# Optimization experiments

Hardware: AMD Instinct MI355X
Metric: run time of the kernel (lower is better)

Reference implementation:

```python
import jax, jax.numpy as jnp
import numpy as np

NEG = -1e9  # effectively -inf for masked logits, grad-safe

def apply_rope(t, cos, sin):
    # t: [b, H, S, D]; cos/sin: [S, D] -> rotate-half RoPE
    d = t.shape[-1]
    t1, t2 = t[..., : d // 2], t[..., d // 2 :]
    rot = jnp.concatenate([-t2, t1], axis=-1)
    return t * cos[None, None] + rot * sin[None, None]


def setup_inputs() -> dict:
    key = jax.random.key(0)
    ks = jax.random.split(key, 8)
    b, S, d_in = 1, 4096, 2048
    H, G, D = 16, 4, 128
    d_out = H * D
    sc = 1.0 / np.sqrt(d_in)
    x = jax.random.normal(ks[0], (b, S, d_in), dtype=jnp.float32)
    # causal mask: True = masked (future positions)
    mask = jnp.triu(jnp.ones((S, S), dtype=bool), k=1)
    inv = 1.0 / (10000.0 ** (jnp.arange(0, D, 2, dtype=jnp.float32) / D))
    ang = jnp.arange(S, dtype=jnp.float32)[:, None] * inv[None, :]  # [S, D/2]
    ang = jnp.concatenate([ang, ang], axis=-1)                      # [S, D]
    cos, sin = jnp.cos(ang), jnp.sin(ang)
    Wq = jax.random.normal(ks[1], (d_out, d_in), dtype=jnp.float32) * sc
    Wk = jax.random.normal(ks[2], (G * D, d_in), dtype=jnp.float32) * sc
    Wv = jax.random.normal(ks[3], (G * D, d_in), dtype=jnp.float32) * sc
    Wo = jax.random.normal(ks[4], (d_in, d_out), dtype=jnp.float32) * sc
    return {"x": x, "mask": mask, "cos": cos, "sin": sin,
            "Wq": Wq, "Wk": Wk, "Wv": Wv, "Wo": Wo}


def reference(x, mask, cos, sin, Wq, Wk, Wv, Wo):
    b, S, d_in = x.shape
    G = Wk.shape[0] // cos.shape[-1]          # num_kv_groups
    D = cos.shape[-1]                          # head_dim
    H = Wq.shape[0] // D                       # num_heads
    n = H // G                                 # group_size
    q = (x @ Wq.T).reshape(b, S, H, D).transpose(0, 2, 1, 3)   # [b,H,S,D]
    k = (x @ Wk.T).reshape(b, S, G, D).transpose(0, 2, 1, 3)   # [b,G,S,D]
    v = (x @ Wv.T).reshape(b, S, G, D).transpose(0, 2, 1, 3)
    q = apply_rope(q, cos, sin)
    k = apply_rope(k, cos, sin)
    # GQA: group heads instead of repeat_interleave (head h -> group h // n)
    qg = q.reshape(b, G, n, S, D)
    scores = jnp.einsum('bgnqd,bgkd->bgnqk', qg, k)            # [b,G,n,S,S]
    scores = jnp.where(mask[None, None, None], NEG, scores)
    w = jax.nn.softmax(scores / np.sqrt(D), axis=-1)
    ctx = jnp.einsum('bgnqk,bgkd->bgnqd', w, v)                # [b,G,n,S,D]
    ctx = ctx.reshape(b, H, S, D).transpose(0, 2, 1, 3).reshape(b, S, H * D)
    return ctx @ Wo.T
```

## Files before the change

kernel.cpp:

```cpp
#include <hip/hip_runtime.h>

typedef __attribute__((ext_vector_type(8))) short bf16x8;
typedef __attribute__((ext_vector_type(4))) short bf16x4;
typedef __attribute__((ext_vector_type(8))) unsigned short u16x8;
typedef __attribute__((ext_vector_type(4))) float f32x4;

__device__ __forceinline__ unsigned short f2b(float f) {
  unsigned int u = __builtin_bit_cast(unsigned int, f);
  u += 0x7FFFu + ((u >> 16) & 1u);
  return (unsigned short)(u >> 16);
}
__device__ __forceinline__ float b2f(unsigned short h) {
  return __builtin_bit_cast(float, ((unsigned int)h) << 16);
}

__device__ __forceinline__ f32x4 mfma16x16x16(bf16x4 a, bf16x4 b, f32x4 c) {
#if __has_builtin(__builtin_amdgcn_mfma_f32_16x16x16bf16_1k)
  return __builtin_amdgcn_mfma_f32_16x16x16bf16_1k(a, b, c, 0, 0, 0);
#else
  asm volatile("v_mfma_f32_16x16x16_bf16 %0, %1, %2, %0" : "+v"(c) : "v"(a), "v"(b));
  return c;
#endif
}

#define AS1(p) (const __attribute__((address_space(1))) void*)(p)
#define AS3(p) (__attribute__((address_space(3))) void*)(p)

__global__ __launch_bounds__(256) void k_cvt(const float* __restrict__ in,
                                             unsigned short* __restrict__ out,
                                             float scale) {
  int i = blockIdx.x * 256 + threadIdx.x;
  const float4* p = (const float4*)in + (size_t)i * 2;
  float4 a = p[0], b = p[1];
  u16x8 r;
  r[0] = f2b(a.x * scale); r[1] = f2b(a.y * scale);
  r[2] = f2b(a.z * scale); r[3] = f2b(a.w * scale);
  r[4] = f2b(b.x * scale); r[5] = f2b(b.y * scale);
  r[6] = f2b(b.z * scale); r[7] = f2b(b.w * scale);
  *((u16x8*)out + i) = r;
}

__global__ __launch_bounds__(256) void k_rope(unsigned short* __restrict__ qk,
                                              const float* __restrict__ cosb,
                                              const float* __restrict__ sinb) {
  int tid = blockIdx.x * 256 + threadIdx.x;
  int oct = tid & 7;
  int hd  = (tid >> 3) % 20;
  int s   = (tid >> 3) / 20;
  unsigned short* p1 = qk + (size_t)s * 3072 + hd * 128 + oct * 8;
  unsigned short* p2 = p1 + 64;
  u16x8 a = *(const u16x8*)p1;
  u16x8 b = *(const u16x8*)p2;
  const float4* cp = (const float4*)(cosb + (size_t)s * 128 + oct * 8);
  const float4* sp = (const float4*)(sinb + (size_t)s * 128 + oct * 8);
  float4 c0 = cp[0], c1 = cp[1], s0 = sp[0], s1 = sp[1];
  float cs[8] = {c0.x,c0.y,c0.z,c0.w,c1.x,c1.y,c1.z,c1.w};
  float sn[8] = {s0.x,s0.y,s0.z,s0.w,s1.x,s1.y,s1.z,s1.w};
  u16x8 ra, rb;
#pragma unroll
  for (int j = 0; j < 8; ++j) {
    float av = b2f(a[j]), bv = b2f(b[j]);
    ra[j] = f2b(av * cs[j] - bv * sn[j]);
    rb[j] = f2b(bv * cs[j] + av * sn[j]);
  }
  *(u16x8*)p1 = ra;
  *(u16x8*)p2 = rb;
}

__global__ __launch_bounds__(256) void k_tr(const unsigned short* __restrict__ src,
                                            unsigned short* __restrict__ dst) {
  __shared__ unsigned short tile[64][72];
  const int bs = blockIdx.x, bc = blockIdx.y, t = threadIdx.x;
#pragma unroll
  for (int i = 0; i < 2; ++i) {
    int c8 = t + 256 * i;
    int row = c8 >> 3, cb = c8 & 7;
    u16x8 v = *(const u16x8*)(src + (size_t)(bs * 64 + row) * 3072 + 2560 + bc * 64 + cb * 8);
#pragma unroll
    for (int j = 0; j < 8; ++j) tile[row][cb * 8 + j] = v[j];
  }
  __syncthreads();
#pragma unroll
  for (int i = 0; i < 2; ++i) {
    int c8 = t + 256 * i;
    int crow = c8 >> 3, sb = c8 & 7;
    u16x8 v;
#pragma unroll
    for (int j = 0; j < 8; ++j) v[j] = tile[sb * 8 + j][crow];
    *(u16x8*)(dst + (size_t)(bc * 64 + crow) * 4096 + bs * 64 + sb * 8) = v;
  }
}

template <int OUTF32>
__global__ __launch_bounds__(256) void k_gemm_bt(
    const unsigned short* __restrict__ A, const unsigned short* __restrict__ B,
    void* __restrict__ C, int K, int lda, int ldb, int ldc) {
  __shared__ unsigned short As[128 * 64];
  __shared__ unsigned short Bs[128 * 64];
  const int t = threadIdx.x;
  const int lane = t & 63, w = t >> 6;
  const int wm = w >> 1, wn = w & 1;
  const int bn = blockIdx.x, bm = blockIdx.y;
  const unsigned short* Arow = A + (size_t)(bm * 128) * lda;
  const unsigned short* Brow = B + (size_t)(bn * 128) * ldb;

  f32x4 acc[4][4] = {};
  for (int kt = 0; kt < K; kt += 64) {
#pragma unroll
    for (int i = 0; i < 4; ++i) {
      int idx = i * 256 + t;
      int r = idx >> 3, blk = idx & 7;
      int sb = blk ^ (r & 7);
      __builtin_amdgcn_global_load_lds(AS1(Arow + (size_t)r * lda + kt + sb * 8),
                                       AS3(As + (i * 256 + w * 64) * 8), 16, 0, 0);
    }
#pragma unroll
    for (int i = 0; i < 4; ++i) {
      int idx = i * 256 + t;
      int r = idx >> 3, blk = idx & 7;
      int sb = blk ^ (r & 7);
      __builtin_amdgcn_global_load_lds(AS1(Brow + (size_t)r * ldb + kt + sb * 8),
                                       AS3(Bs + (i * 256 + w * 64) * 8), 16, 0, 0);
    }
    __syncthreads();
#pragma unroll
    for (int kk = 0; kk < 2; ++kk) {
      bf16x8 av[4], bv[4];
#pragma unroll
      for (int i = 0; i < 4; ++i) {
        int r = wm * 64 + i * 16 + (lane & 15);
        int off = (r * 128 + (kk * 32 + (lane >> 4) * 8) * 2) ^ ((r & 7) << 4);
        av[i] = *(const bf16x8*)((const char*)As + off);
      }
#pragma unroll
      for (int j = 0; j < 4; ++j) {
        int r = wn * 64 + j * 16 + (lane & 15);
        int off = (r * 128 + (kk * 32 + (lane >> 4) * 8) * 2) ^ ((r & 7) << 4);
        bv[j] = *(const bf16x8*)((const char*)Bs + off);
      }
#pragma unroll
      for (int i = 0; i < 4; ++i)
#pragma unroll
        for (int j = 0; j < 4; ++j)
          acc[i][j] = __builtin_amdgcn_mfma_f32_16x16x32_bf16(av[i], bv[j], acc[i][j], 0, 0, 0);
    }
    __syncthreads();
  }
#pragma unroll
  for (int i = 0; i < 4; ++i)
#pragma unroll
    for (int j = 0; j < 4; ++j)
#pragma unroll
      for (int r = 0; r < 4; ++r) {
        int m = bm * 128 + wm * 64 + i * 16 + (lane >> 4) * 4 + r;
        int n = bn * 128 + wn * 64 + j * 16 + (lane & 15);
        float v = acc[i][j][r];
        if (OUTF32) ((float*)C)[(size_t)m * ldc + n] = v;
        else        ((unsigned short*)C)[(size_t)m * ldc + n] = f2b(v);
      }
}

__device__ __forceinline__ void stage_k(const unsigned short* __restrict__ qk,
                                        unsigned short* __restrict__ dst,
                                        int kt, int g, int t, int w) {
#pragma unroll
  for (int i = 0; i < 4; ++i) {
    int idx = i * 256 + t;
    int r = idx >> 4, blk = idx & 15;
    int sb = (blk & 8) | ((blk ^ r) & 7);
    __builtin_amdgcn_global_load_lds(
        AS1(qk + (size_t)(kt * 64 + r) * 3072 + 2048 + g * 128 + sb * 8),
        AS3(dst + (i * 256 + w * 64) * 8), 16, 0, 0);
  }
}
__device__ __forceinline__ void stage_v(const unsigned short* __restrict__ vT,
                                        unsigned short* __restrict__ dst,
                                        int kt, int g, int t, int w) {
#pragma unroll
  for (int i = 0; i < 4; ++i) {
    int idx = i * 256 + t;
    int r = idx >> 3, blk = idx & 7;
    int sb = blk ^ (r & 7);
    __builtin_amdgcn_global_load_lds(
        AS1(vT + (size_t)(g * 128 + r) * 4096 + kt * 64 + sb * 8),
        AS3(dst + (i * 256 + w * 64) * 8), 16, 0, 0);
  }
}

__global__ __launch_bounds__(256, 2) void k_attn(const unsigned short* __restrict__ qk,
                                                 const unsigned short* __restrict__ vT,
                                                 unsigned short* __restrict__ ctx) {
  __shared__ unsigned short Ks[2][64 * 128];
  __shared__ unsigned short Vs[2][64 * 128];
  const int b = blockIdx.x, h = blockIdx.y, g = h >> 2;
  const int t = threadIdx.x, lane = t & 63, w = t >> 6;
  const int l15 = lane & 15, lq = lane >> 4;

  for (int ph = 0; ph < 2; ++ph) {
    const int qt = ph ? 63 - b : b;
    const int qg = qt * 64 + w * 16 + l15;

    bf16x8 aq[4];
    {
      const unsigned short* qb =
          qk + (size_t)(qt * 64 + w * 16 + l15) * 3072 + h * 128 + lq * 8;
#pragma unroll
      for (int sl = 0; sl < 4; ++sl) aq[sl] = *(const bf16x8*)(qb + sl * 32);
    }
    f32x4 o[8] = {};
    float lsum = 0.f;

    stage_k(qk, Ks[0], 0, g, t, w);
    stage_v(vT, Vs[0], 0, g, t, w);
    asm volatile("s_waitcnt vmcnt(0)" ::: "memory");
    __builtin_amdgcn_s_barrier();

    auto tile = [&](const unsigned short* Kb, const unsigned short* Vb,
                    int kt, bool maskT) {
      f32x4 st[4] = {};
      __builtin_amdgcn_s_setprio(1);
#pragma unroll
      for (int sl = 0; sl < 4; ++sl)
#pragma unroll
        for (int nt = 0; nt < 4; ++nt) {
          int key = nt * 16 + l15;
          int off = (key * 256 + sl * 64 + lq * 16) ^ ((key & 7) << 4);
          bf16x8 bk = *(const bf16x8*)((const char*)Kb + off);
          st[nt] = __builtin_amdgcn_mfma_f32_16x16x32_bf16(bk, aq[sl], st[nt], 0, 0, 0);
        }
      __builtin_amdgcn_s_setprio(0);

      bf16x4 pa[4];
#pragma unroll
      for (int nt = 0; nt < 4; ++nt)
#pragma unroll
        for (int r = 0; r < 4; ++r) {
          float p = __builtin_amdgcn_exp2f(st[nt][r]);
          if (maskT) {
            int key = kt * 64 + nt * 16 + lq * 4 + r;
            if (key > qg) p = 0.f;
          }
          lsum += p;
          unsigned int u = __builtin_bit_cast(unsigned int, p) + 0x8000u;
          pa[nt][r] = (short)(u >> 16);
        }

      __builtin_amdgcn_s_setprio(1);
#pragma unroll
      for (int nt = 0; nt < 4; ++nt)
#pragma unroll
        for (int dt = 0; dt < 8; ++dt) {
          int d = dt * 16 + l15;
          int off = (d * 128 + nt * 32 + lq * 8) ^ ((d & 7) << 4);
          bf16x4 vv = *(const bf16x4*)((const char*)Vb + off);
          o[dt] = mfma16x16x16(pa[nt], vv, o[dt]);
        }
      __builtin_amdgcn_s_setprio(0);
    };

    for (int kt = 0; kt < qt; ++kt) {
      const int cur = kt & 1;
      stage_k(qk, Ks[cur ^ 1], kt + 1, g, t, w);
      stage_v(vT, Vs[cur ^ 1], kt + 1, g, t, w);
      tile(Ks[cur], Vs[cur], kt, false);
      asm volatile("s_waitcnt vmcnt(0)" ::: "memory");
      __builtin_amdgcn_s_barrier();
    }
    {
      const int cur = qt & 1;
      tile(Ks[cur], Vs[cur], qt, true);
      __builtin_amdgcn_s_barrier();
    }

    float fs = lsum;
    fs += __shfl_xor(fs, 16);
    fs += __shfl_xor(fs, 32);
    float invq[4];
#pragma unroll
    for (int r = 0; r < 4; ++r) invq[r] = 1.f / __shfl(fs, lq * 4 + r);
#pragma unroll
    for (int dt = 0; dt < 8; ++dt)
#pragma unroll
      for (int r = 0; r < 4; ++r) {
        int q = qt * 64 + w * 16 + lq * 4 + r;
        int c = h * 128 + dt * 16 + l15;
        ctx[(size_t)q * 2048 + c] = f2b(o[dt][r] * invq[r]);
      }
  }
}

extern "C" void kernel_launch(void* const* d_in, const int* in_sizes, int n_in,
                              void* d_out, int out_size, void* d_ws, size_t ws_size,
                              hipStream_t stream) {
  const float* x    = (const float*)d_in[0];
  const float* cosb = (const float*)d_in[2];
  const float* sinb = (const float*)d_in[3];
  const float* Wq   = (const float*)d_in[4];
  const float* Wk   = (const float*)d_in[5];
  const float* Wv   = (const float*)d_in[6];
  const float* Wo   = (const float*)d_in[7];

  char* p = (char*)d_ws;
  unsigned short* xb   = (unsigned short*)p; p += (size_t)8388608 * 2;
  unsigned short* wqkv = (unsigned short*)p; p += (size_t)6291456 * 2;
  unsigned short* Wob  = (unsigned short*)p; p += (size_t)4194304 * 2;
  unsigned short* qkvb = (unsigned short*)p; p += (size_t)4096 * 3072 * 2;
  unsigned short* vTb  = (unsigned short*)p; p += (size_t)512 * 4096 * 2;
  unsigned short* ctx  = (unsigned short*)p; p += (size_t)4096 * 2048 * 2;
  if (ws_size < (size_t)(p - (char*)d_ws)) return;

  const float SC = 0.12751741f;

  k_cvt<<<4096, 256, 0, stream>>>(x,  xb, 1.f);
  k_cvt<<<2048, 256, 0, stream>>>(Wq, wqkv,           SC);
  k_cvt<<< 512, 256, 0, stream>>>(Wk, wqkv + 4194304, 1.f);
  k_cvt<<< 512, 256, 0, stream>>>(Wv, wqkv + 5242880, 1.f);
  k_cvt<<<2048, 256, 0, stream>>>(Wo, Wob, 1.f);

  k_gemm_bt<0><<<dim3(24, 32), 256, 0, stream>>>(xb, wqkv, qkvb, 2048, 2048, 2048, 3072);

  k_rope<<<2560, 256, 0, stream>>>(qkvb, cosb, sinb);
  k_tr<<<dim3(64, 8), 256, 0, stream>>>(qkvb, vTb);

  k_attn<<<dim3(32, 16), 256, 0, stream>>>(qkvb, vTb, ctx);

  k_gemm_bt<1><<<dim3(16, 32), 256, 0, stream>>>(ctx, Wob, d_out, 2048, 2048, 2048, 2048);
}
```

Measured before the change: 255.1 us.

## Merge conversion and post-GEMM launches and streamline the attention inner loop

The five fp32-to-bf16 conversion launches become one kernel that picks its source from the block index. RoPE and the V transpose are merged into a single launch, and they touch disjoint column ranges. In attention, the K/V staging pointers and swizzled LDS offsets are computed once and then incremented each tile. Probabilities are packed with v_cvt_pk_bf16_f32, and the softmax row sum comes from an extra MFMA against a ones vector instead of scalar adds and shuffles. The aim is less launch overhead and fewer VALU instructions per tile, at the cost of one extra MFMA per key sub-tile and a row sum taken from bf16-rounded probabilities.

```diff
diff --git a/kernel.cpp b/kernel.cpp
--- a/kernel.cpp
+++ b/kernel.cpp
@@ -4,6 +4,7 @@
 typedef __attribute__((ext_vector_type(4))) short bf16x4;
 typedef __attribute__((ext_vector_type(8))) unsigned short u16x8;
 typedef __attribute__((ext_vector_type(4))) float f32x4;
+typedef __attribute__((ext_vector_type(2))) unsigned int u32x2;
 
 __device__ __forceinline__ unsigned short f2b(float f) {
   unsigned int u = __builtin_bit_cast(unsigned int, f);
@@ -23,13 +24,20 @@
 #endif
 }
 
+__device__ __forceinline__ bf16x4 pack4(float a, float b, float c, float d) {
+  unsigned int lo, hi;
+  asm("v_cvt_pk_bf16_f32 %0, %1, %2" : "=v"(lo) : "v"(a), "v"(b));
+  asm("v_cvt_pk_bf16_f32 %0, %1, %2" : "=v"(hi) : "v"(c), "v"(d));
+  u32x2 u = {lo, hi};
+  return __builtin_bit_cast(bf16x4, u);
+}
+
 #define AS1(p) (const __attribute__((address_space(1))) void*)(p)
 #define AS3(p) (__attribute__((address_space(3))) void*)(p)
 
-__global__ __launch_bounds__(256) void k_cvt(const float* __restrict__ in,
-                                             unsigned short* __restrict__ out,
-                                             float scale) {
-  int i = blockIdx.x * 256 + threadIdx.x;
+__device__ __forceinline__ void cvt8(const float* __restrict__ in,
+                                     unsigned short* __restrict__ out,
+                                     int i, float scale) {
   const float4* p = (const float4*)in + (size_t)i * 2;
   float4 a = p[0], b = p[1];
   u16x8 r;
@@ -40,54 +48,71 @@
   *((u16x8*)out + i) = r;
 }
 
-__global__ __launch_bounds__(256) void k_rope(unsigned short* __restrict__ qk,
+__global__ __launch_bounds__(256) void k_cvt_all(
+    const float* __restrict__ x,  const float* __restrict__ Wq,
+    const float* __restrict__ Wk, const float* __restrict__ Wv,
+    const float* __restrict__ Wo, unsigned short* __restrict__ xb,
+    unsigned short* __restrict__ wqkv, unsigned short* __restrict__ Wob,
+    float sc) {
+  int bid = blockIdx.x;
+  int tid = threadIdx.x;
+  if (bid < 4096)      cvt8(x,  xb,             (bid        ) * 256 + tid, 1.f);
+  else if (bid < 6144) cvt8(Wq, wqkv,           (bid - 4096) * 256 + tid, sc);
+  else if (bid < 6656) cvt8(Wk, wqkv + 4194304, (bid - 6144) * 256 + tid, 1.f);
+  else if (bid < 7168) cvt8(Wv, wqkv + 5242880, (bid - 6656) * 256 + tid, 1.f);
+  else                 cvt8(Wo, Wob,            (bid - 7168) * 256 + tid, 1.f);
+}
+
+__global__ __launch_bounds__(256) void k_post(unsigned short* __restrict__ qkv,
                                               const float* __restrict__ cosb,
-                                              const float* __restrict__ sinb) {
-  int tid = blockIdx.x * 256 + threadIdx.x;
-  int oct = tid & 7;
-  int hd  = (tid >> 3) % 20;
-  int s   = (tid >> 3) / 20;
-  unsigned short* p1 = qk + (size_t)s * 3072 + hd * 128 + oct * 8;
-  unsigned short* p2 = p1 + 64;
-  u16x8 a = *(const u16x8*)p1;
-  u16x8 b = *(const u16x8*)p2;
-  const float4* cp = (const float4*)(cosb + (size_t)s * 128 + oct * 8);
-  const float4* sp = (const float4*)(sinb + (size_t)s * 128 + oct * 8);
-  float4 c0 = cp[0], c1 = cp[1], s0 = sp[0], s1 = sp[1];
-  float cs[8] = {c0.x,c0.y,c0.z,c0.w,c1.x,c1.y,c1.z,c1.w};
-  float sn[8] = {s0.x,s0.y,s0.z,s0.w,s1.x,s1.y,s1.z,s1.w};
-  u16x8 ra, rb;
-#pragma unroll
-  for (int j = 0; j < 8; ++j) {
-    float av = b2f(a[j]), bv = b2f(b[j]);
-    ra[j] = f2b(av * cs[j] - bv * sn[j]);
-    rb[j] = f2b(bv * cs[j] + av * sn[j]);
-  }
-  *(u16x8*)p1 = ra;
-  *(u16x8*)p2 = rb;
-}
-
-__global__ __launch_bounds__(256) void k_tr(const unsigned short* __restrict__ src,
-                                            unsigned short* __restrict__ dst) {
+                                              const float* __restrict__ sinb,
+                                              unsigned short* __restrict__ vT) {
   __shared__ unsigned short tile[64][72];
-  const int bs = blockIdx.x, bc = blockIdx.y, t = threadIdx.x;
-#pragma unroll
-  for (int i = 0; i < 2; ++i) {
-    int c8 = t + 256 * i;
-    int row = c8 >> 3, cb = c8 & 7;
-    u16x8 v = *(const u16x8*)(src + (size_t)(bs * 64 + row) * 3072 + 2560 + bc * 64 + cb * 8);
-#pragma unroll
-    for (int j = 0; j < 8; ++j) tile[row][cb * 8 + j] = v[j];
-  }
-  __syncthreads();
-#pragma unroll
-  for (int i = 0; i < 2; ++i) {
-    int c8 = t + 256 * i;
-    int crow = c8 >> 3, sb = c8 & 7;
-    u16x8 v;
-#pragma unroll
-    for (int j = 0; j < 8; ++j) v[j] = tile[sb * 8 + j][crow];
-    *(u16x8*)(dst + (size_t)(bc * 64 + crow) * 4096 + bs * 64 + sb * 8) = v;
+  const int bid = blockIdx.x, t = threadIdx.x;
+  if (bid < 2560) {
+    int tid = bid * 256 + t;
+    int oct = tid & 7;
+    int hd  = (tid >> 3) % 20;
+    int s   = (tid >> 3) / 20;
+    unsigned short* p1 = qkv + (size_t)s * 3072 + hd * 128 + oct * 8;
+    unsigned short* p2 = p1 + 64;
+    u16x8 a = *(const u16x8*)p1;
+    u16x8 b = *(const u16x8*)p2;
+    const float4* cp = (const float4*)(cosb + (size_t)s * 128 + oct * 8);
+    const float4* sp = (const float4*)(sinb + (size_t)s * 128 + oct * 8);
+    float4 c0 = cp[0], c1 = cp[1], s0 = sp[0], s1 = sp[1];
+    float cs[8] = {c0.x,c0.y,c0.z,c0.w,c1.x,c1.y,c1.z,c1.w};
+    float sn[8] = {s0.x,s0.y,s0.z,s0.w,s1.x,s1.y,s1.z,s1.w};
+    u16x8 ra, rb;
+#pragma unroll
+    for (int j = 0; j < 8; ++j) {
+      float av = b2f(a[j]), bv = b2f(b[j]);
+      ra[j] = f2b(av * cs[j] - bv * sn[j]);
+      rb[j] = f2b(bv * cs[j] + av * sn[j]);
+    }
+    *(u16x8*)p1 = ra;
+    *(u16x8*)p2 = rb;
+  } else {
+    int idx = bid - 2560;
+    int bs = idx >> 3, bc = idx & 7;
+#pragma unroll
+    for (int i = 0; i < 2; ++i) {
+      int c8 = t + 256 * i;
+      int row = c8 >> 3, cb = c8 & 7;
+      u16x8 v = *(const u16x8*)(qkv + (size_t)(bs * 64 + row) * 3072 + 2560 + bc * 64 + cb * 8);
+#pragma unroll
+      for (int j = 0; j < 8; ++j) tile[row][cb * 8 + j] = v[j];
+    }
+    __syncthreads();
+#pragma unroll
+    for (int i = 0; i < 2; ++i) {
+      int c8 = t + 256 * i;
+      int crow = c8 >> 3, sb = c8 & 7;
+      u16x8 v;
+#pragma unroll
+      for (int j = 0; j < 8; ++j) v[j] = tile[sb * 8 + j][crow];
+      *(u16x8*)(vT + (size_t)(bc * 64 + crow) * 4096 + bs * 64 + sb * 8) = v;
+    }
   }
 }
 
@@ -160,33 +185,6 @@
       }
 }
 
-__device__ __forceinline__ void stage_k(const unsigned short* __restrict__ qk,
-                                        unsigned short* __restrict__ dst,
-                                        int kt, int g, int t, int w) {
-#pragma unroll
-  for (int i = 0; i < 4; ++i) {
-    int idx = i * 256 + t;
-    int r = idx >> 4, blk = idx & 15;
-    int sb = (blk & 8) | ((blk ^ r) & 7);
-    __builtin_amdgcn_global_load_lds(
-        AS1(qk + (size_t)(kt * 64 + r) * 3072 + 2048 + g * 128 + sb * 8),
-        AS3(dst + (i * 256 + w * 64) * 8), 16, 0, 0);
-  }
-}
-__device__ __forceinline__ void stage_v(const unsigned short* __restrict__ vT,
-                                        unsigned short* __restrict__ dst,
-                                        int kt, int g, int t, int w) {
-#pragma unroll
-  for (int i = 0; i < 4; ++i) {
-    int idx = i * 256 + t;
-    int r = idx >> 3, blk = idx & 7;
-    int sb = blk ^ (r & 7);
-    __builtin_amdgcn_global_load_lds(
-        AS1(vT + (size_t)(g * 128 + r) * 4096 + kt * 64 + sb * 8),
-        AS3(dst + (i * 256 + w * 64) * 8), 16, 0, 0);
-  }
-}
-
 __global__ __launch_bounds__(256, 2) void k_attn(const unsigned short* __restrict__ qk,
                                                  const unsigned short* __restrict__ vT,
                                                  unsigned short* __restrict__ ctx) {
@@ -195,10 +193,36 @@
   const int b = blockIdx.x, h = blockIdx.y, g = h >> 2;
   const int t = threadIdx.x, lane = t & 63, w = t >> 6;
   const int l15 = lane & 15, lq = lane >> 4;
+  const int xv = (l15 & 7) << 4;
+
+  int kb[4], vb[4];
+#pragma unroll
+  for (int sl = 0; sl < 4; ++sl) kb[sl] = ((sl * 64 + lq * 16) ^ xv) + l15 * 256;
+#pragma unroll
+  for (int nt = 0; nt < 4; ++nt) vb[nt] = ((nt * 32 + lq * 8) ^ xv) + l15 * 128;
+
+  const bf16x4 ones = { (short)0x3F80, (short)0x3F80, (short)0x3F80, (short)0x3F80 };
 
   for (int ph = 0; ph < 2; ++ph) {
     const int qt = ph ? 63 - b : b;
     const int qg = qt * 64 + w * 16 + l15;
+
+    const unsigned short* kgp[4];
+    const unsigned short* vgp[4];
+    unsigned short* kld[4];
+    unsigned short* vld[4];
+#pragma unroll
+    for (int i = 0; i < 4; ++i) {
+      int idx = i * 256 + t;
+      int r = idx >> 4, blk = idx & 15;
+      int sb = (blk & 8) | ((blk ^ r) & 7);
+      kgp[i] = qk + (size_t)r * 3072 + 2048 + g * 128 + sb * 8;
+      kld[i] = (unsigned short*)Ks[0] + (size_t)(i * 256 + w * 64) * 8;
+      int r2 = idx >> 3, blk2 = idx & 7;
+      int sb2 = blk2 ^ (r2 & 7);
+      vgp[i] = vT + (size_t)(g * 128 + r2) * 4096 + sb2 * 8;
+      vld[i] = (unsigned short*)Vs[0] + (size_t)(i * 256 + w * 64) * 8;
+    }
 
     bf16x8 aq[4];
     {
@@ -208,76 +232,102 @@
       for (int sl = 0; sl < 4; ++sl) aq[sl] = *(const bf16x8*)(qb + sl * 32);
     }
     f32x4 o[8] = {};
-    float lsum = 0.f;
-
-    stage_k(qk, Ks[0], 0, g, t, w);
-    stage_v(vT, Vs[0], 0, g, t, w);
+    f32x4 osum = {};
+    bf16x4 pa[4];
+
+#pragma unroll
+    for (int i = 0; i < 4; ++i) {
+      __builtin_amdgcn_global_load_lds(AS1(kgp[i]), AS3(kld[i]), 16, 0, 0);
+      __builtin_amdgcn_global_load_lds(AS1(vgp[i]), AS3(vld[i]), 16, 0, 0);
+      kgp[i] += 64 * 3072;
+      vgp[i] += 64;
+    }
     asm volatile("s_waitcnt vmcnt(0)" ::: "memory");
     __builtin_amdgcn_s_barrier();
 
-    auto tile = [&](const unsigned short* Kb, const unsigned short* Vb,
-                    int kt, bool maskT) {
+    for (int kt = 0; kt < qt; ++kt) {
+      const int cur = kt & 1, nb = cur ^ 1;
+      const char* Kc = (const char*)Ks[cur];
+      const char* Vc = (const char*)Vs[cur];
+#pragma unroll
+      for (int i = 0; i < 4; ++i) {
+        __builtin_amdgcn_global_load_lds(AS1(kgp[i]), AS3(kld[i] + nb * 8192), 16, 0, 0);
+        __builtin_amdgcn_global_load_lds(AS1(vgp[i]), AS3(vld[i] + nb * 8192), 16, 0, 0);
+        kgp[i] += 64 * 3072;
+        vgp[i] += 64;
+      }
       f32x4 st[4] = {};
       __builtin_amdgcn_s_setprio(1);
 #pragma unroll
       for (int sl = 0; sl < 4; ++sl)
 #pragma unroll
         for (int nt = 0; nt < 4; ++nt) {
-          int key = nt * 16 + l15;
-          int off = (key * 256 + sl * 64 + lq * 16) ^ ((key & 7) << 4);
-          bf16x8 bk = *(const bf16x8*)((const char*)Kb + off);
+          bf16x8 bk = *(const bf16x8*)(Kc + kb[sl] + nt * 4096);
           st[nt] = __builtin_amdgcn_mfma_f32_16x16x32_bf16(bk, aq[sl], st[nt], 0, 0, 0);
         }
       __builtin_amdgcn_s_setprio(0);
-
-      bf16x4 pa[4];
-#pragma unroll
-      for (int nt = 0; nt < 4; ++nt)
-#pragma unroll
-        for (int r = 0; r < 4; ++r) {
-          float p = __builtin_amdgcn_exp2f(st[nt][r]);
-          if (maskT) {
-            int key = kt * 64 + nt * 16 + lq * 4 + r;
-            if (key > qg) p = 0.f;
-          }
-          lsum += p;
-          unsigned int u = __builtin_bit_cast(unsigned int, p) + 0x8000u;
-          pa[nt][r] = (short)(u >> 16);
-        }
-
+#pragma unroll
+      for (int nt = 0; nt < 4; ++nt) {
+        float p0 = __builtin_amdgcn_exp2f(st[nt][0]);
+        float p1 = __builtin_amdgcn_exp2f(st[nt][1]);
+        float p2 = __builtin_amdgcn_exp2f(st[nt][2]);
+        float p3 = __builtin_amdgcn_exp2f(st[nt][3]);
+        pa[nt] = pack4(p0, p1, p2, p3);
+      }
       __builtin_amdgcn_s_setprio(1);
 #pragma unroll
-      for (int nt = 0; nt < 4; ++nt)
+      for (int nt = 0; nt < 4; ++nt) {
+        osum = mfma16x16x16(pa[nt], ones, osum);
 #pragma unroll
         for (int dt = 0; dt < 8; ++dt) {
-          int d = dt * 16 + l15;
-          int off = (d * 128 + nt * 32 + lq * 8) ^ ((d & 7) << 4);
-          bf16x4 vv = *(const bf16x4*)((const char*)Vb + off);
+          bf16x4 vv = *(const bf16x4*)(Vc + vb[nt] + dt * 2048);
           o[dt] = mfma16x16x16(pa[nt], vv, o[dt]);
         }
+      }
       __builtin_amdgcn_s_setprio(0);
-    };
-
-    for (int kt = 0; kt < qt; ++kt) {
-      const int cur = kt & 1;
-      stage_k(qk, Ks[cur ^ 1], kt + 1, g, t, w);
-      stage_v(vT, Vs[cur ^ 1], kt + 1, g, t, w);
-      tile(Ks[cur], Vs[cur], kt, false);
       asm volatile("s_waitcnt vmcnt(0)" ::: "memory");
       __builtin_amdgcn_s_barrier();
     }
     {
-      const int cur = qt & 1;
-      tile(Ks[cur], Vs[cur], qt, true);
+      const char* Kc = (const char*)Ks[qt & 1];
+      const char* Vc = (const char*)Vs[qt & 1];
+      f32x4 st[4] = {};
+      __builtin_amdgcn_s_setprio(1);
+#pragma unroll
+      for (int sl = 0; sl < 4; ++sl)
+#pragma unroll
+        for (int nt = 0; nt < 4; ++nt) {
+          bf16x8 bk = *(const bf16x8*)(Kc + kb[sl] + nt * 4096);
+          st[nt] = __builtin_amdgcn_mfma_f32_16x16x32_bf16(bk, aq[sl], st[nt], 0, 0, 0);
+        }
+      __builtin_amdgcn_s_setprio(0);
+#pragma unroll
+      for (int nt = 0; nt < 4; ++nt) {
+        float pp[4];
+#pragma unroll
+        for (int r = 0; r < 4; ++r) {
+          int key = qt * 64 + nt * 16 + lq * 4 + r;
+          pp[r] = (key > qg) ? 0.f : __builtin_amdgcn_exp2f(st[nt][r]);
+        }
+        pa[nt] = pack4(pp[0], pp[1], pp[2], pp[3]);
+      }
+      __builtin_amdgcn_s_setprio(1);
+#pragma unroll
+      for (int nt = 0; nt < 4; ++nt) {
+        osum = mfma16x16x16(pa[nt], ones, osum);
+#pragma unroll
+        for (int dt = 0; dt < 8; ++dt) {
+          bf16x4 vv = *(const bf16x4*)(Vc + vb[nt] + dt * 2048);
+          o[dt] = mfma16x16x16(pa[nt], vv, o[dt]);
+        }
+      }
+      __builtin_amdgcn_s_setprio(0);
       __builtin_amdgcn_s_barrier();
     }
 
-    float fs = lsum;
-    fs += __shfl_xor(fs, 16);
-    fs += __shfl_xor(fs, 32);
     float invq[4];
 #pragma unroll
-    for (int r = 0; r < 4; ++r) invq[r] = 1.f / __shfl(fs, lq * 4 + r);
+    for (int r = 0; r < 4; ++r) invq[r] = 1.f / osum[r];
 #pragma unroll
     for (int dt = 0; dt < 8; ++dt)
 #pragma unroll
@@ -311,16 +361,11 @@
 
   const float SC = 0.12751741f;
 
-  k_cvt<<<4096, 256, 0, stream>>>(x,  xb, 1.f);
-  k_cvt<<<2048, 256, 0, stream>>>(Wq, wqkv,           SC);
-  k_cvt<<< 512, 256, 0, stream>>>(Wk, wqkv + 4194304, 1.f);
-  k_cvt<<< 512, 256, 0, stream>>>(Wv, wqkv + 5242880, 1.f);
-  k_cvt<<<2048, 256, 0, stream>>>(Wo, Wob, 1.f);
+  k_cvt_all<<<9216, 256, 0, stream>>>(x, Wq, Wk, Wv, Wo, xb, wqkv, Wob, SC);
 
   k_gemm_bt<0><<<dim3(24, 32), 256, 0, stream>>>(xb, wqkv, qkvb, 2048, 2048, 2048, 3072);
 
-  k_rope<<<2560, 256, 0, stream>>>(qkvb, cosb, sinb);
-  k_tr<<<dim3(64, 8), 256, 0, stream>>>(qkvb, vTb);
+  k_post<<<3072, 256, 0, stream>>>(qkvb, cosb, sinb, vTb);
 
   k_attn<<<dim3(32, 16), 256, 0, stream>>>(qkvb, vTb, ctx);
 
```

New measurement: 261.4 us. 2.5% more time.
